# Kernel tuning notes

Measured on AMD Instinct MI355X. Metric: run time of the kernel, lower is better.

The kernel has to match this reference:

```python
import jax, jax.numpy as jnp
import numpy as np

B, H, S, D = 2, 12, 1024, 128
KQ, KK = 6, 11  # per-head conv kernel over (query, key) score plane


def setup_inputs() -> dict:
    key = jax.random.key(0)
    kq, kk, kv, kw = jax.random.split(key, 4)
    Q = jax.random.normal(kq, (B, H, S, D), dtype=jnp.float32)
    K = jax.random.normal(kk, (B, H, S, D), dtype=jnp.float32)
    V = jax.random.normal(kv, (B, H, S, D), dtype=jnp.float32)
    W = jax.random.normal(kw, (H, KQ, KK), dtype=jnp.float32) * 0.1
    return {"Q": Q, "K": K, "V": V, "W": W}


def reference(Q, K, V, W):
    # causal=True, softmax_scale = 1/sqrt(head_dim)  (module defaults)
    b, h, s, d = Q.shape
    _, kq, kk = W.shape
    pad_q = kq - 1            # causal padding along the query axis
    pad_k = (kk - 1) // 2     # 'same' padding along the key axis
    scale = 1.0 / np.sqrt(d).astype(np.float32)

    # Raw QK^T scores: [b, h, s_q, s_k]
    scores = jnp.einsum('bhqd,bhkd->bhqk', Q, K)

    # Causal: zero out future keys before the conv so the kernel cannot mix
    # in future information (matches the `causal` flag passed into the
    # fused qk_conv kernel; out-of-range tiles load as 0 in the Triton code).
    tril = jnp.tril(jnp.ones((s, s), dtype=bool))
    scores = jnp.where(tril[None, None], scores, 0.0)

    # Per-head 2D conv over the (q, k) plane: grouped conv with H groups,
    # kernel W[h] applied to head h's score map. Cross-correlation (PyTorch
    # conv semantics == lax.conv_general_dilated without kernel flip).
    conv = jax.lax.conv_general_dilated(
        scores,                      # [b, h, s, s] as NCHW
        W[:, None, :, :],            # [h, 1, kq, kk] as OIHW, groups=h
        window_strides=(1, 1),
        padding=((pad_q, 0), (pad_k, pad_k)),
        feature_group_count=h,
        dimension_numbers=('NCHW', 'OIHW', 'NCHW'),
    )

    # Scale, re-apply causal mask with the kernel's -1e6 fill, softmax, @V.
    logits = conv * scale + jnp.where(tril[None, None], 0.0, -1000000.0)
    P = jax.nn.softmax(logits, axis=-1)
    O = jnp.einsum('bhqk,bhkd->bhqd', P, V)
    return O
```

## Files before the change

### kernel.cpp

```cpp
#include <hip/hip_runtime.h>
#include <hip/hip_bf16.h>
#include <math.h>

#define B_ 2
#define H_ 12
#define S_ 1024
#define D_ 128
#define TQ 64
#define TK 32
#define SCALE 0.08838834764831843f

#define QROWS (S_ + 16)
#define KROWS (16 + S_ + 16)

#define QBLK 3120
#define KBLK 3168
#define VBLK 3072

#define SCW 56

typedef __attribute__((ext_vector_type(8))) short short8;
typedef __attribute__((ext_vector_type(4))) float floatx4;

__device__ __forceinline__ unsigned short f2b(float f) {
    return __builtin_bit_cast(unsigned short, __float2bfloat16(f));
}

__global__ __launch_bounds__(256) void prep_kernel(
    const float* __restrict__ Q, const float* __restrict__ K,
    const float* __restrict__ V,
    unsigned short* __restrict__ Qp, unsigned short* __restrict__ Kp,
    unsigned short* __restrict__ Vt)
{
    __shared__ float ls[32][33];
    const int bid = blockIdx.x;
    const int tid = threadIdx.x;
    if (bid < QBLK) {
        int e0 = (bid * 256 + tid) * 4;
        int bh = e0 / (QROWS * D_);
        int rem = e0 - bh * (QROWS * D_);
        int r = rem >> 7, d = rem & 127;
        int sr = r - 16;
        float4 v = make_float4(0.f, 0.f, 0.f, 0.f);
        if (sr >= 0 && sr < S_) v = *(const float4*)(Q + ((size_t)bh * S_ + sr) * D_ + d);
        ushort4 o; o.x = f2b(v.x); o.y = f2b(v.y); o.z = f2b(v.z); o.w = f2b(v.w);
        *(ushort4*)(Qp + ((size_t)bh * QROWS + r) * D_ + d) = o;
    } else if (bid < QBLK + KBLK) {
        int e0 = ((bid - QBLK) * 256 + tid) * 4;
        int bh = e0 / (KROWS * D_);
        int rem = e0 - bh * (KROWS * D_);
        int r = rem >> 7, d = rem & 127;
        int sr = r - 16;
        float4 v = make_float4(0.f, 0.f, 0.f, 0.f);
        if (sr >= 0 && sr < S_) v = *(const float4*)(K + ((size_t)bh * S_ + sr) * D_ + d);
        ushort4 o; o.x = f2b(v.x); o.y = f2b(v.y); o.z = f2b(v.z); o.w = f2b(v.w);
        *(ushort4*)(Kp + ((size_t)bh * KROWS + r) * D_ + d) = o;
    } else {
        int b = bid - (QBLK + KBLK);
        int dt = b & 3; int kt = (b >> 2) & 31; int bh = b >> 7;
        int lk = tid >> 3, ld = (tid & 7) * 4;
        float4 v = *(const float4*)(V + ((size_t)bh * S_ + kt * 32 + lk) * D_ + dt * 32 + ld);
        ls[lk][ld + 0] = v.x; ls[lk][ld + 1] = v.y; ls[lk][ld + 2] = v.z; ls[lk][ld + 3] = v.w;
        __syncthreads();
        int lk2 = tid >> 3, lc = (tid & 7) * 4;
        ushort4 o;
        o.x = f2b(ls[lc + 0][lk2]); o.y = f2b(ls[lc + 1][lk2]);
        o.z = f2b(ls[lc + 2][lk2]); o.w = f2b(ls[lc + 3][lk2]);
        *(ushort4*)(Vt + ((size_t)bh * D_ + dt * 32 + lk2) * S_ + kt * 32 + lc) = o;
    }
}

__global__ __launch_bounds__(256, 2) void conv_attn_mfma(
    const unsigned short* __restrict__ Qp,
    const unsigned short* __restrict__ Kp,
    const unsigned short* __restrict__ Vt,
    const float* __restrict__ W,
    float* __restrict__ O)
{
    __shared__ __align__(16) unsigned short Qs[80][136];
    __shared__ __align__(16) unsigned short sc[2][80][SCW];
    __shared__ __align__(16) unsigned short Pst[4][16][40];
    __shared__ float Wf[66];

    const int tid = threadIdx.x;
    const int wv = tid >> 6;
    const int ln = tid & 63;
    const int l15 = ln & 15;
    const int qd = ln >> 4;

    const int bid = blockIdx.x;
    const int bh = (bid & 7) * 3 + ((bid >> 3) % 3);
    const int g = bid / 24;
    const int qt = (g & 1) ? (g >> 1) : (15 - (g >> 1));
    const int h = bh % H_;
    const int q0 = qt * TQ;

    const unsigned short* Qb = Qp + (size_t)bh * QROWS * D_;
    const unsigned short* Kb = Kp + (size_t)bh * KROWS * D_;
    const unsigned short* Vb = Vt + (size_t)bh * D_ * S_;

    if (tid < 66) Wf[tid] = W[h * 66 + tid];

    for (int idx = tid; idx < 80 * 16; idx += 256) {
        int r = idx >> 4, c8 = (idx & 15) * 8;
        *(short8*)&Qs[r][c8] = *(const short8*)(Qb + (size_t)(q0 + r) * D_ + c8);
    }
    __syncthreads();

    short8 bfr[6];
    #pragma unroll
    for (int i = 0; i < 6; ++i) {
        short8 b;
        #pragma unroll
        for (int j = 0; j < 8; ++j) {
            int widx = qd * 8 + j - l15 - 3;
            float v = (widx >= 0 && widx <= 10) ? Wf[i * 11 + widx] : 0.f;
            b[j] = (short)f2b(v);
        }
        bfr[i] = b;
    }

    const int nu = (wv == 3) ? 3 : 4;
    int nt_t[4], mt_t[4];
    #pragma unroll
    for (int t = 0; t < 4; ++t) {
        int u = wv * 4 + t;
        if (u > 14) u = 14;
        nt_t[t] = u / 5; mt_t[t] = u - (u / 5) * 5;
    }

    floatx4 acc[8];
    #pragma unroll
    for (int nt = 0; nt < 8; ++nt) acc[nt] = (floatx4){0.f, 0.f, 0.f, 0.f};
    float m_run[4] = {-INFINITY, -INFINITY, -INFINITY, -INFINITY};
    float l_run[4] = {0.f, 0.f, 0.f, 0.f};

    const int nkt = 2 * qt + 2;
    for (int kt = 0; kt < nkt; ++kt) {
        const int k0 = kt * TK;
        const int buf = kt & 1;

        for (int t = 0; t < nu; ++t) {
            const int nt = nt_t[t], mt = mt_t[t];
            const unsigned short* krow = Kb + (size_t)(k0 + 8 + nt * 16 + l15) * D_;
            floatx4 s = {0.f, 0.f, 0.f, 0.f};
            #pragma unroll
            for (int kc = 0; kc < 4; ++kc) {
                short8 kf = *(const short8*)(krow + kc * 32 + qd * 8);
                short8 qf = *(const short8*)&Qs[mt * 16 + l15][kc * 32 + qd * 8];
                s = __builtin_amdgcn_mfma_f32_16x16x32_bf16(qf, kf, s, 0, 0, 0);
            }
            const int qrow = q0 - 16 + mt * 16 + qd * 4;
            const int kcol = k0 - 8 + nt * 16 + l15;
            #pragma unroll
            for (int reg = 0; reg < 4; ++reg)
                sc[buf][mt * 16 + qd * 4 + reg][nt * 16 + l15] =
                    (kcol <= qrow + reg) ? f2b(s[reg]) : (unsigned short)0;
        }
        __syncthreads();

        floatx4 cv[2];
        #pragma unroll
        for (int n = 0; n < 2; ++n) {
            floatx4 c4 = {0.f, 0.f, 0.f, 0.f};
            #pragma unroll
            for (int i = 0; i < 6; ++i) {
                short8 af = *(const short8*)&sc[buf][wv * 16 + l15 + 11 + i][n * 16 + qd * 8];
                c4 = __builtin_amdgcn_mfma_f32_16x16x32_bf16(af, bfr[i], c4, 0, 0, 0);
            }
            cv[n] = c4;
        }

        float lg[2][4];
        #pragma unroll
        for (int n = 0; n < 2; ++n)
            #pragma unroll
            for (int reg = 0; reg < 4; ++reg) {
                const int q = q0 + wv * 16 + qd * 4 + reg;
                const int k = k0 + n * 16 + l15;
                lg[n][reg] = (k <= q) ? cv[n][reg] * SCALE : -1e30f;
            }
        float alpha[4];
        float p[2][4];
        #pragma unroll
        for (int reg = 0; reg < 4; ++reg) {
            float mx = fmaxf(lg[0][reg], lg[1][reg]);
            mx = fmaxf(mx, __shfl_xor(mx, 1));
            mx = fmaxf(mx, __shfl_xor(mx, 2));
            mx = fmaxf(mx, __shfl_xor(mx, 4));
            mx = fmaxf(mx, __shfl_xor(mx, 8));
            const float nm = fmaxf(m_run[reg], mx);
            alpha[reg] = __expf(m_run[reg] - nm);
            p[0][reg] = __expf(lg[0][reg] - nm);
            p[1][reg] = __expf(lg[1][reg] - nm);
            float sum = p[0][reg] + p[1][reg];
            sum += __shfl_xor(sum, 1);
            sum += __shfl_xor(sum, 2);
            sum += __shfl_xor(sum, 4);
            sum += __shfl_xor(sum, 8);
            l_run[reg] = l_run[reg] * alpha[reg] + sum;
            m_run[reg] = nm;
        }

        #pragma unroll
        for (int n = 0; n < 2; ++n)
            #pragma unroll
            for (int reg = 0; reg < 4; ++reg)
                Pst[wv][qd * 4 + reg][n * 16 + l15] = f2b(p[n][reg]);

        #pragma unroll
        for (int nt = 0; nt < 8; ++nt)
            #pragma unroll
            for (int reg = 0; reg < 4; ++reg)
                acc[nt][reg] *= alpha[reg];

        {
            short8 pf = *(const short8*)&Pst[wv][l15][qd * 8];
            #pragma unroll
            for (int nt = 0; nt < 8; ++nt) {
                short8 vf = *(const short8*)(Vb + (size_t)(nt * 16 + l15) * S_ + k0 + qd * 8);
                acc[nt] = __builtin_amdgcn_mfma_f32_16x16x32_bf16(pf, vf, acc[nt], 0, 0, 0);
            }
        }
    }

    {
        float inv[4];
        #pragma unroll
        for (int reg = 0; reg < 4; ++reg) inv[reg] = 1.0f / l_run[reg];
        float* Ob = O + (size_t)bh * S_ * D_;
        #pragma unroll
        for (int reg = 0; reg < 4; ++reg) {
            const int row = q0 + wv * 16 + qd * 4 + reg;
            #pragma unroll
            for (int nt = 0; nt < 8; ++nt)
                Ob[(size_t)row * D_ + nt * 16 + l15] = acc[nt][reg] * inv[reg];
        }
    }
}

extern "C" void kernel_launch(void* const* d_in, const int* in_sizes, int n_in,
                              void* d_out, int out_size, void* d_ws, size_t ws_size,
                              hipStream_t stream) {
    const float* Q = (const float*)d_in[0];
    const float* K = (const float*)d_in[1];
    const float* V = (const float*)d_in[2];
    const float* W = (const float*)d_in[3];
    float* O = (float*)d_out;

    unsigned short* Qp = (unsigned short*)d_ws;
    unsigned short* Kp = (unsigned short*)((char*)d_ws + 6389760);
    unsigned short* Vt = (unsigned short*)((char*)d_ws + 12877824);

    prep_kernel<<<dim3(QBLK + KBLK + VBLK), dim3(256), 0, stream>>>(Q, K, V, Qp, Kp, Vt);
    conv_attn_mfma<<<dim3(B_ * H_ * (S_ / TQ)), dim3(256), 0, stream>>>(Qp, Kp, Vt, W, O);
}
```

Measured before the change: 244.6 us.

## Split key tiles across waves with split-K softmax merge and smaller query tiles

The query tile shrinks from 64 to 32 rows, so the grid doubles, and each of the four waves now handles a strided subset of key tiles for all 32 query rows instead of its own 16 rows. That removes the per-iteration block barrier and the shared score double buffer. Per-wave running max and sum are merged at the end through shared memory, and outputs are reduced there too before a coalesced float4 store. Q is converted to bf16 inside the attention kernel, which drops the Q prep pass and its workspace. The cost is a serialized cross-wave reduction at the end, recomputed score halos per wave, and higher register use under the launch bound of 3 blocks.

```diff
diff --git a/kernel.cpp b/kernel.cpp
--- a/kernel.cpp
+++ b/kernel.cpp
@@ -6,19 +6,14 @@
 #define H_ 12
 #define S_ 1024
 #define D_ 128
-#define TQ 64
+#define TQ 32
 #define TK 32
 #define SCALE 0.08838834764831843f
 
-#define QROWS (S_ + 16)
 #define KROWS (16 + S_ + 16)
-
-#define QBLK 3120
 #define KBLK 3168
 #define VBLK 3072
 
-#define SCW 56
-
 typedef __attribute__((ext_vector_type(8))) short short8;
 typedef __attribute__((ext_vector_type(4))) float floatx4;
 
@@ -27,26 +22,14 @@
 }
 
 __global__ __launch_bounds__(256) void prep_kernel(
-    const float* __restrict__ Q, const float* __restrict__ K,
-    const float* __restrict__ V,
-    unsigned short* __restrict__ Qp, unsigned short* __restrict__ Kp,
-    unsigned short* __restrict__ Vt)
+    const float* __restrict__ K, const float* __restrict__ V,
+    unsigned short* __restrict__ Kp, unsigned short* __restrict__ Vt)
 {
     __shared__ float ls[32][33];
     const int bid = blockIdx.x;
     const int tid = threadIdx.x;
-    if (bid < QBLK) {
+    if (bid < KBLK) {
         int e0 = (bid * 256 + tid) * 4;
-        int bh = e0 / (QROWS * D_);
-        int rem = e0 - bh * (QROWS * D_);
-        int r = rem >> 7, d = rem & 127;
-        int sr = r - 16;
-        float4 v = make_float4(0.f, 0.f, 0.f, 0.f);
-        if (sr >= 0 && sr < S_) v = *(const float4*)(Q + ((size_t)bh * S_ + sr) * D_ + d);
-        ushort4 o; o.x = f2b(v.x); o.y = f2b(v.y); o.z = f2b(v.z); o.w = f2b(v.w);
-        *(ushort4*)(Qp + ((size_t)bh * QROWS + r) * D_ + d) = o;
-    } else if (bid < QBLK + KBLK) {
-        int e0 = ((bid - QBLK) * 256 + tid) * 4;
         int bh = e0 / (KROWS * D_);
         int rem = e0 - bh * (KROWS * D_);
         int r = rem >> 7, d = rem & 127;
@@ -56,7 +39,7 @@
         ushort4 o; o.x = f2b(v.x); o.y = f2b(v.y); o.z = f2b(v.z); o.w = f2b(v.w);
         *(ushort4*)(Kp + ((size_t)bh * KROWS + r) * D_ + d) = o;
     } else {
-        int b = bid - (QBLK + KBLK);
+        int b = bid - KBLK;
         int dt = b & 3; int kt = (b >> 2) & 31; int bh = b >> 7;
         int lk = tid >> 3, ld = (tid & 7) * 4;
         float4 v = *(const float4*)(V + ((size_t)bh * S_ + kt * 32 + lk) * D_ + dt * 32 + ld);
@@ -70,16 +53,20 @@
     }
 }
 
-__global__ __launch_bounds__(256, 2) void conv_attn_mfma(
-    const unsigned short* __restrict__ Qp,
+__global__ __launch_bounds__(256, 3) void conv_attn_mfma(
+    const float* __restrict__ Q,
     const unsigned short* __restrict__ Kp,
     const unsigned short* __restrict__ Vt,
     const float* __restrict__ W,
     float* __restrict__ O)
 {
-    __shared__ __align__(16) unsigned short Qs[80][136];
-    __shared__ __align__(16) unsigned short sc[2][80][SCW];
-    __shared__ __align__(16) unsigned short Pst[4][16][40];
+    __shared__ __align__(16) unsigned short Qs[48][136];
+    __shared__ __align__(16) union {
+        unsigned short sc[4][48][56];
+        float oacc[32][132];
+    } u;
+    __shared__ __align__(16) unsigned short Pst[4][32][40];
+    __shared__ float m_all[4][32], l_all[4][32], ms_s[32], inv_s[32];
     __shared__ float Wf[66];
 
     const int tid = threadIdx.x;
@@ -91,19 +78,20 @@
     const int bid = blockIdx.x;
     const int bh = (bid & 7) * 3 + ((bid >> 3) % 3);
     const int g = bid / 24;
-    const int qt = (g & 1) ? (g >> 1) : (15 - (g >> 1));
+    const int qt = (g & 1) ? (g >> 1) : (31 - (g >> 1));
     const int h = bh % H_;
     const int q0 = qt * TQ;
 
-    const unsigned short* Qb = Qp + (size_t)bh * QROWS * D_;
-    const unsigned short* Kb = Kp + (size_t)bh * KROWS * D_;
-    const unsigned short* Vb = Vt + (size_t)bh * D_ * S_;
-
     if (tid < 66) Wf[tid] = W[h * 66 + tid];
 
-    for (int idx = tid; idx < 80 * 16; idx += 256) {
-        int r = idx >> 4, c8 = (idx & 15) * 8;
-        *(short8*)&Qs[r][c8] = *(const short8*)(Qb + (size_t)(q0 + r) * D_ + c8);
+    const float* Qb = Q + (size_t)bh * S_ * D_;
+    for (int idx = tid; idx < 48 * 32; idx += 256) {
+        int r = idx >> 5, c4 = (idx & 31) * 4;
+        int row = q0 - 16 + r;
+        float4 v = make_float4(0.f, 0.f, 0.f, 0.f);
+        if (row >= 0) v = *(const float4*)(Qb + (size_t)row * D_ + c4);
+        ushort4 o; o.x = f2b(v.x); o.y = f2b(v.y); o.z = f2b(v.z); o.w = f2b(v.w);
+        *(ushort4*)&Qs[r][c4] = o;
     }
     __syncthreads();
 
@@ -120,121 +108,170 @@
         bfr[i] = b;
     }
 
-    const int nu = (wv == 3) ? 3 : 4;
-    int nt_t[4], mt_t[4];
+    const unsigned short* Kb = Kp + (size_t)bh * KROWS * D_;
+    const unsigned short* Vb = Vt + (size_t)bh * D_ * S_;
+
+    floatx4 acc[2][8];
     #pragma unroll
-    for (int t = 0; t < 4; ++t) {
-        int u = wv * 4 + t;
-        if (u > 14) u = 14;
-        nt_t[t] = u / 5; mt_t[t] = u - (u / 5) * 5;
-    }
-
-    floatx4 acc[8];
+    for (int m2 = 0; m2 < 2; ++m2)
+        #pragma unroll
+        for (int nt = 0; nt < 8; ++nt)
+            acc[m2][nt] = (floatx4){0.f, 0.f, 0.f, 0.f};
+    float m_run[2][4], l_run[2][4];
     #pragma unroll
-    for (int nt = 0; nt < 8; ++nt) acc[nt] = (floatx4){0.f, 0.f, 0.f, 0.f};
-    float m_run[4] = {-INFINITY, -INFINITY, -INFINITY, -INFINITY};
-    float l_run[4] = {0.f, 0.f, 0.f, 0.f};
-
-    const int nkt = 2 * qt + 2;
-    for (int kt = 0; kt < nkt; ++kt) {
+    for (int m2 = 0; m2 < 2; ++m2)
+        #pragma unroll
+        for (int reg = 0; reg < 4; ++reg) { m_run[m2][reg] = -INFINITY; l_run[m2][reg] = 0.f; }
+
+    for (int kt = wv; kt <= qt; kt += 4) {
         const int k0 = kt * TK;
-        const int buf = kt & 1;
-
-        for (int t = 0; t < nu; ++t) {
-            const int nt = nt_t[t], mt = mt_t[t];
+
+        #pragma unroll
+        for (int nt = 0; nt < 3; ++nt) {
             const unsigned short* krow = Kb + (size_t)(k0 + 8 + nt * 16 + l15) * D_;
-            floatx4 s = {0.f, 0.f, 0.f, 0.f};
-            #pragma unroll
-            for (int kc = 0; kc < 4; ++kc) {
-                short8 kf = *(const short8*)(krow + kc * 32 + qd * 8);
-                short8 qf = *(const short8*)&Qs[mt * 16 + l15][kc * 32 + qd * 8];
-                s = __builtin_amdgcn_mfma_f32_16x16x32_bf16(qf, kf, s, 0, 0, 0);
-            }
-            const int qrow = q0 - 16 + mt * 16 + qd * 4;
-            const int kcol = k0 - 8 + nt * 16 + l15;
-            #pragma unroll
-            for (int reg = 0; reg < 4; ++reg)
-                sc[buf][mt * 16 + qd * 4 + reg][nt * 16 + l15] =
-                    (kcol <= qrow + reg) ? f2b(s[reg]) : (unsigned short)0;
-        }
-        __syncthreads();
-
-        floatx4 cv[2];
-        #pragma unroll
-        for (int n = 0; n < 2; ++n) {
-            floatx4 c4 = {0.f, 0.f, 0.f, 0.f};
-            #pragma unroll
-            for (int i = 0; i < 6; ++i) {
-                short8 af = *(const short8*)&sc[buf][wv * 16 + l15 + 11 + i][n * 16 + qd * 8];
-                c4 = __builtin_amdgcn_mfma_f32_16x16x32_bf16(af, bfr[i], c4, 0, 0, 0);
-            }
-            cv[n] = c4;
-        }
-
-        float lg[2][4];
-        #pragma unroll
-        for (int n = 0; n < 2; ++n)
+            short8 kf[4];
+            #pragma unroll
+            for (int kc = 0; kc < 4; ++kc)
+                kf[kc] = *(const short8*)(krow + kc * 32 + qd * 8);
+            #pragma unroll
+            for (int mt = 0; mt < 3; ++mt) {
+                floatx4 s = {0.f, 0.f, 0.f, 0.f};
+                #pragma unroll
+                for (int kc = 0; kc < 4; ++kc) {
+                    short8 qf = *(const short8*)&Qs[mt * 16 + l15][kc * 32 + qd * 8];
+                    s = __builtin_amdgcn_mfma_f32_16x16x32_bf16(qf, kf[kc], s, 0, 0, 0);
+                }
+                const int qrow = q0 - 16 + mt * 16 + qd * 4;
+                const int kcol = k0 - 8 + nt * 16 + l15;
+                #pragma unroll
+                for (int reg = 0; reg < 4; ++reg)
+                    u.sc[wv][mt * 16 + qd * 4 + reg][nt * 16 + l15] =
+                        (kcol <= qrow + reg) ? f2b(s[reg]) : (unsigned short)0;
+            }
+        }
+
+        floatx4 cv[2][2];
+        #pragma unroll
+        for (int m2 = 0; m2 < 2; ++m2)
+            #pragma unroll
+            for (int n = 0; n < 2; ++n) {
+                floatx4 c4 = {0.f, 0.f, 0.f, 0.f};
+                #pragma unroll
+                for (int i = 0; i < 6; ++i) {
+                    short8 af = *(const short8*)&u.sc[wv][m2 * 16 + l15 + 11 + i][n * 16 + qd * 8];
+                    c4 = __builtin_amdgcn_mfma_f32_16x16x32_bf16(af, bfr[i], c4, 0, 0, 0);
+                }
+                cv[m2][n] = c4;
+            }
+
+        float alpha[2][4];
+        #pragma unroll
+        for (int m2 = 0; m2 < 2; ++m2) {
             #pragma unroll
             for (int reg = 0; reg < 4; ++reg) {
-                const int q = q0 + wv * 16 + qd * 4 + reg;
-                const int k = k0 + n * 16 + l15;
-                lg[n][reg] = (k <= q) ? cv[n][reg] * SCALE : -1e30f;
-            }
-        float alpha[4];
-        float p[2][4];
-        #pragma unroll
-        for (int reg = 0; reg < 4; ++reg) {
-            float mx = fmaxf(lg[0][reg], lg[1][reg]);
-            mx = fmaxf(mx, __shfl_xor(mx, 1));
-            mx = fmaxf(mx, __shfl_xor(mx, 2));
-            mx = fmaxf(mx, __shfl_xor(mx, 4));
-            mx = fmaxf(mx, __shfl_xor(mx, 8));
-            const float nm = fmaxf(m_run[reg], mx);
-            alpha[reg] = __expf(m_run[reg] - nm);
-            p[0][reg] = __expf(lg[0][reg] - nm);
-            p[1][reg] = __expf(lg[1][reg] - nm);
-            float sum = p[0][reg] + p[1][reg];
-            sum += __shfl_xor(sum, 1);
-            sum += __shfl_xor(sum, 2);
-            sum += __shfl_xor(sum, 4);
-            sum += __shfl_xor(sum, 8);
-            l_run[reg] = l_run[reg] * alpha[reg] + sum;
-            m_run[reg] = nm;
-        }
-
-        #pragma unroll
-        for (int n = 0; n < 2; ++n)
-            #pragma unroll
-            for (int reg = 0; reg < 4; ++reg)
-                Pst[wv][qd * 4 + reg][n * 16 + l15] = f2b(p[n][reg]);
-
-        #pragma unroll
-        for (int nt = 0; nt < 8; ++nt)
-            #pragma unroll
-            for (int reg = 0; reg < 4; ++reg)
-                acc[nt][reg] *= alpha[reg];
+                const int q = q0 + m2 * 16 + qd * 4 + reg;
+                float lg0 = (k0 + l15 <= q)      ? cv[m2][0][reg] * SCALE : -1e30f;
+                float lg1 = (k0 + 16 + l15 <= q) ? cv[m2][1][reg] * SCALE : -1e30f;
+                float mx = fmaxf(lg0, lg1);
+                mx = fmaxf(mx, __shfl_xor(mx, 1));
+                mx = fmaxf(mx, __shfl_xor(mx, 2));
+                mx = fmaxf(mx, __shfl_xor(mx, 4));
+                mx = fmaxf(mx, __shfl_xor(mx, 8));
+                const float nm = fmaxf(m_run[m2][reg], mx);
+                alpha[m2][reg] = __expf(m_run[m2][reg] - nm);
+                float p0 = __expf(lg0 - nm);
+                float p1 = __expf(lg1 - nm);
+                float sum = p0 + p1;
+                sum += __shfl_xor(sum, 1);
+                sum += __shfl_xor(sum, 2);
+                sum += __shfl_xor(sum, 4);
+                sum += __shfl_xor(sum, 8);
+                l_run[m2][reg] = l_run[m2][reg] * alpha[m2][reg] + sum;
+                m_run[m2][reg] = nm;
+                Pst[wv][m2 * 16 + qd * 4 + reg][l15]      = f2b(p0);
+                Pst[wv][m2 * 16 + qd * 4 + reg][16 + l15] = f2b(p1);
+            }
+        }
+
+        #pragma unroll
+        for (int m2 = 0; m2 < 2; ++m2)
+            #pragma unroll
+            for (int reg = 0; reg < 4; ++reg) {
+                const float a = alpha[m2][reg];
+                #pragma unroll
+                for (int nt = 0; nt < 8; ++nt)
+                    acc[m2][nt][reg] *= a;
+            }
 
         {
-            short8 pf = *(const short8*)&Pst[wv][l15][qd * 8];
+            short8 pf[2];
+            #pragma unroll
+            for (int m2 = 0; m2 < 2; ++m2)
+                pf[m2] = *(const short8*)&Pst[wv][m2 * 16 + l15][qd * 8];
             #pragma unroll
             for (int nt = 0; nt < 8; ++nt) {
                 short8 vf = *(const short8*)(Vb + (size_t)(nt * 16 + l15) * S_ + k0 + qd * 8);
-                acc[nt] = __builtin_amdgcn_mfma_f32_16x16x32_bf16(pf, vf, acc[nt], 0, 0, 0);
-            }
-        }
+                #pragma unroll
+                for (int m2 = 0; m2 < 2; ++m2)
+                    acc[m2][nt] = __builtin_amdgcn_mfma_f32_16x16x32_bf16(pf[m2], vf, acc[m2][nt], 0, 0, 0);
+            }
+        }
+    }
+
+    if (l15 == 0) {
+        #pragma unroll
+        for (int m2 = 0; m2 < 2; ++m2)
+            #pragma unroll
+            for (int reg = 0; reg < 4; ++reg) {
+                const int r = m2 * 16 + qd * 4 + reg;
+                m_all[wv][r] = m_run[m2][reg];
+                l_all[wv][r] = l_run[m2][reg];
+            }
+    }
+    __syncthreads();
+    if (tid < 32) {
+        float ms = -INFINITY;
+        #pragma unroll
+        for (int w = 0; w < 4; ++w) ms = fmaxf(ms, m_all[w][tid]);
+        float ls = 0.f;
+        #pragma unroll
+        for (int w = 0; w < 4; ++w) ls += __expf(m_all[w][tid] - ms) * l_all[w][tid];
+        ms_s[tid] = ms;
+        inv_s[tid] = 1.f / ls;
+    }
+    __syncthreads();
+    for (int w = 0; w < 4; ++w) {
+        if (wv == w) {
+            #pragma unroll
+            for (int m2 = 0; m2 < 2; ++m2)
+                #pragma unroll
+                for (int reg = 0; reg < 4; ++reg) {
+                    const int r = m2 * 16 + qd * 4 + reg;
+                    const float f = __expf(m_run[m2][reg] - ms_s[r]);
+                    #pragma unroll
+                    for (int nt = 0; nt < 8; ++nt) {
+                        const float val = acc[m2][nt][reg] * f;
+                        if (w == 0) u.oacc[r][nt * 16 + l15] = val;
+                        else        u.oacc[r][nt * 16 + l15] += val;
+                    }
+                }
+        }
+        __syncthreads();
     }
 
     {
-        float inv[4];
-        #pragma unroll
-        for (int reg = 0; reg < 4; ++reg) inv[reg] = 1.0f / l_run[reg];
-        float* Ob = O + (size_t)bh * S_ * D_;
-        #pragma unroll
-        for (int reg = 0; reg < 4; ++reg) {
-            const int row = q0 + wv * 16 + qd * 4 + reg;
-            #pragma unroll
-            for (int nt = 0; nt < 8; ++nt)
-                Ob[(size_t)row * D_ + nt * 16 + l15] = acc[nt][reg] * inv[reg];
+        const int r = tid >> 3;
+        const int c0 = (tid & 7) * 16;
+        const float inv = inv_s[r];
+        float* orow = O + ((size_t)bh * S_ + q0 + r) * D_ + c0;
+        #pragma unroll
+        for (int g4 = 0; g4 < 4; ++g4) {
+            float4 o;
+            o.x = u.oacc[r][c0 + g4 * 4 + 0] * inv;
+            o.y = u.oacc[r][c0 + g4 * 4 + 1] * inv;
+            o.z = u.oacc[r][c0 + g4 * 4 + 2] * inv;
+            o.w = u.oacc[r][c0 + g4 * 4 + 3] * inv;
+            *(float4*)(orow + g4 * 4) = o;
         }
     }
 }
@@ -248,10 +285,9 @@
     const float* W = (const float*)d_in[3];
     float* O = (float*)d_out;
 
-    unsigned short* Qp = (unsigned short*)d_ws;
-    unsigned short* Kp = (unsigned short*)((char*)d_ws + 6389760);
-    unsigned short* Vt = (unsigned short*)((char*)d_ws + 12877824);
-
-    prep_kernel<<<dim3(QBLK + KBLK + VBLK), dim3(256), 0, stream>>>(Q, K, V, Qp, Kp, Vt);
-    conv_attn_mfma<<<dim3(B_ * H_ * (S_ / TQ)), dim3(256), 0, stream>>>(Qp, Kp, Vt, W, O);
-}
+    unsigned short* Kp = (unsigned short*)d_ws;
+    unsigned short* Vt = (unsigned short*)((char*)d_ws + 6488064);
+
+    prep_kernel<<<dim3(KBLK + VBLK), dim3(256), 0, stream>>>(K, V, Kp, Vt);
+    conv_attn_mfma<<<dim3(B_ * H_ * (S_ / TQ)), dim3(256), 0, stream>>>(Q, Kp, Vt, W, O);
+}
```

Result: faster. 202.0 us (-17.4%).
